# Kernel optimization log

Hardware: AMD Instinct MI355X
Metric: run time of the kernel (lower is better)

## Reference

```python
import jax, jax.numpy as jnp
import numpy as np

N, E, D_IN, H = 40000, 640000, 128, 128
R, B = 8, 30  # num_relations = 2*n_speakers**2, num_bases


def setup_inputs() -> dict:
    key = jax.random.key(0)
    ks = jax.random.split(key, 10)
    node_features = jax.random.normal(ks[0], (N, D_IN), jnp.float32)
    edge_index = jax.random.randint(ks[1], (2, E), 0, N)
    edge_type = jax.random.randint(ks[2], (E,), 0, R)
    edge_norm = jax.random.uniform(ks[3], (E,), jnp.float32)
    s_in = 1.0 / np.sqrt(D_IN)
    s_h = 1.0 / np.sqrt(H)
    basis = jax.random.normal(ks[4], (B, D_IN, H), jnp.float32) * s_in
    comp = jax.random.normal(ks[5], (R, B), jnp.float32) * (1.0 / np.sqrt(B))
    root = jax.random.normal(ks[6], (D_IN, H), jnp.float32) * s_in
    bias1 = jnp.zeros((H,), jnp.float32)
    w_rel = jax.random.normal(ks[7], (H, H), jnp.float32) * s_h
    w_root2 = jax.random.normal(ks[8], (H, H), jnp.float32) * s_h
    bias2 = jnp.zeros((H,), jnp.float32)
    return dict(node_features=node_features, edge_index=edge_index,
                edge_norm=edge_norm, edge_type=edge_type,
                basis=basis, comp=comp, root=root, bias1=bias1,
                w_rel=w_rel, w_root2=w_root2, bias2=bias2)


def reference(node_features, edge_index, edge_norm, edge_type,
              basis, comp, root, bias1, w_rel, w_root2, bias2):
    n = node_features.shape[0]
    src, dst = edge_index[0], edge_index[1]  # messages flow src -> dst

    # ---- RGCNConv (basis decomposition, mean aggregation, root + bias) ----
    # Per-relation weights from bases: [R, D_in, H]
    w = jnp.einsum('rb,bio->rio', comp, basis)
    # Transform all nodes by every relation once (avoids per-edge matmul): [R, N, H]
    xw = jnp.einsum('nd,rdo->rno', node_features, w)
    msgs = xw[edge_type, src]                                  # [E, H]
    agg = jax.ops.segment_sum(msgs, dst, num_segments=n)       # [N, H]
    deg = jax.ops.segment_sum(jnp.ones_like(dst, dtype=node_features.dtype),
                              dst, num_segments=n)
    agg = agg / jnp.maximum(deg, 1.0)[:, None]                 # mean aggregation
    h = agg + node_features @ root + bias1                     # [N, H]

    # ---- GraphConv (add aggregation): W_rel * sum_j x_j + W_root * x_i + b ----
    nbr = jax.ops.segment_sum(h[src], dst, num_segments=n)     # [N, H]
    out = nbr @ w_rel + h @ w_root2 + bias2
    return out
```

## Files before the change

### kernel.cpp

```cpp
#include <hip/hip_runtime.h>
#include <stdint.h>

#define DH 128
#define NB 30
#define NR 8

typedef short bf16x8 __attribute__((ext_vector_type(8)));
typedef float f32x4 __attribute__((ext_vector_type(4)));
typedef float f32x2 __attribute__((ext_vector_type(2)));

static __device__ __forceinline__ unsigned short f2bf(float f) {
    unsigned u = __float_as_uint(f);
    u += 0x7fffu + ((u >> 16) & 1u);
    return (unsigned short)(u >> 16);
}
static __device__ __forceinline__ float bflo(unsigned u) { return __uint_as_float(u << 16); }
static __device__ __forceinline__ float bfhi(unsigned u) { return __uint_as_float(u & 0xffff0000u); }

__global__ __launch_bounds__(256) void k_cvtx(const float* __restrict__ x,
                                              unsigned short* __restrict__ xbf, int n4) {
    int i = blockIdx.x * blockDim.x + threadIdx.x;
    if (i < n4) {
        float4 v = ((const float4*)x)[i];
        ushort4 u;
        u.x = f2bf(v.x); u.y = f2bf(v.y); u.z = f2bf(v.z); u.w = f2bf(v.w);
        ((ushort4*)xbf)[i] = u;
    }
}

__global__ __launch_bounds__(128) void k_wprep(const float* __restrict__ comp,
                                               const float* __restrict__ basis,
                                               const float* __restrict__ root,
                                               const float* __restrict__ wrel,
                                               const float* __restrict__ wroot2,
                                               unsigned short* __restrict__ wallT,
                                               unsigned short* __restrict__ WT2) {
    int o = threadIdx.x;
    int i = blockIdx.x;
    int y = blockIdx.y;
    if (y < NR) {
        float s = 0.f;
        #pragma unroll
        for (int b = 0; b < NB; ++b)
            s += comp[y * NB + b] * basis[((size_t)b * DH + i) * DH + o];
        wallT[((size_t)y * DH + o) * DH + i] = f2bf(s);
    } else if (y == NR) {
        wallT[((size_t)NR * DH + o) * DH + i] = f2bf(root[i * DH + o]);
    } else {
        const float* W = (y == NR + 2) ? wroot2 : wrel;
        WT2[((size_t)(y - NR - 1) * DH + o) * DH + i] = f2bf(W[i * DH + o]);
    }
}

__global__ void k_hist(const int* __restrict__ dst, int E, int* __restrict__ deg) {
    int e = blockIdx.x * blockDim.x + threadIdx.x;
    if (e < E) atomicAdd(&deg[dst[e]], 1);
}

__global__ __launch_bounds__(1024) void k_scan1(const int* __restrict__ deg, int n, int total_n,
                                                int* __restrict__ offsets, int* __restrict__ partial) {
    __shared__ int s[1024];
    int tid = threadIdx.x;
    int i = blockIdx.x * 1024 + tid;
    int v = (i < n) ? deg[i] : 0;
    s[tid] = v;
    __syncthreads();
    for (int off = 1; off < 1024; off <<= 1) {
        int t = (tid >= off) ? s[tid - off] : 0;
        __syncthreads();
        s[tid] += t;
        __syncthreads();
    }
    if (i < total_n) offsets[i] = s[tid] - v;
    if (tid == 1023) partial[blockIdx.x] = s[1023];
}

__global__ void k_scan2(int* __restrict__ partial, int nb) {
    if (threadIdx.x == 0) {
        int run = 0;
        for (int b = 0; b < nb; ++b) { int t = partial[b]; partial[b] = run; run += t; }
    }
}

__global__ __launch_bounds__(1024) void k_scan3(int* __restrict__ offsets,
                                                const int* __restrict__ partial, int total_n) {
    int i = blockIdx.x * 1024 + threadIdx.x;
    if (i < total_n) offsets[i] += partial[blockIdx.x];
}

__global__ void k_scatter(const int* __restrict__ src, const int* __restrict__ dstA,
                          const int* __restrict__ etype, int E,
                          const int* __restrict__ offsets, int* __restrict__ cursor,
                          unsigned* __restrict__ sorted) {
    int e = blockIdx.x * blockDim.x + threadIdx.x;
    if (e >= E) return;
    int d = dstA[e];
    int pos = offsets[d] + atomicAdd(&cursor[d], 1);
    sorted[pos] = (unsigned)src[e] | ((unsigned)etype[e] << 17);
}

__global__ __launch_bounds__(256) void k_gemm1m(const unsigned short* __restrict__ Xbf,
                                                const unsigned short* __restrict__ wallT,
                                                const float* __restrict__ bias1,
                                                int Nn,
                                                unsigned* __restrict__ xw8,
                                                unsigned short* __restrict__ hb) {
    __shared__ __align__(16) unsigned short As[128][136];
    __shared__ __align__(16) unsigned short Bs[128][136];
    const int tid = threadIdx.x;
    const int wave = tid >> 6, lane = tid & 63;
    const int g = blockIdx.y;
    const int rowbase = blockIdx.x * 128;
    const int lq = lane >> 4, lr = lane & 15;

    #pragma unroll
    for (int it = 0; it < 8; ++it) {
        int c = it * 256 + tid;
        int row = c >> 4, col = c & 15;
        int rg = rowbase + row; if (rg >= Nn) rg = Nn - 1;
        *(uint4*)&As[row][col * 8] = *(const uint4*)&Xbf[(size_t)rg * DH + col * 8];
    }

    for (int rr = 0; rr < 3; ++rr) {
        const int r = g * 3 + rr;
        const unsigned short* WT = wallT + (size_t)r * DH * DH;
        if (rr) __syncthreads();
        #pragma unroll
        for (int it = 0; it < 8; ++it) {
            int c = it * 256 + tid;
            int row = c >> 4, col = c & 15;
            *(uint4*)&Bs[row][col * 8] = *(const uint4*)&WT[(size_t)row * DH + col * 8];
        }
        __syncthreads();

        f32x4 acc[2][8];
        #pragma unroll
        for (int mt = 0; mt < 2; ++mt)
            #pragma unroll
            for (int nt = 0; nt < 8; ++nt) acc[mt][nt] = (f32x4)0.f;

        #pragma unroll
        for (int ks = 0; ks < 4; ++ks) {
            const int ko = ks * 32 + lq * 8;
            bf16x8 a0 = *(const bf16x8*)&As[wave * 32 + lr][ko];
            bf16x8 a1 = *(const bf16x8*)&As[wave * 32 + 16 + lr][ko];
            #pragma unroll
            for (int nt = 0; nt < 8; ++nt) {
                bf16x8 b = *(const bf16x8*)&Bs[nt * 16 + lr][ko];
                acc[0][nt] = __builtin_amdgcn_mfma_f32_16x16x32_bf16(a0, b, acc[0][nt], 0, 0, 0);
                acc[1][nt] = __builtin_amdgcn_mfma_f32_16x16x32_bf16(a1, b, acc[1][nt], 0, 0, 0);
            }
        }
        __syncthreads();

        float bv[8];
        #pragma unroll
        for (int nt = 0; nt < 8; ++nt) bv[nt] = (r == NR) ? bias1[nt * 16 + lr] : 0.f;
        #pragma unroll
        for (int mt = 0; mt < 2; ++mt)
            #pragma unroll
            for (int nt = 0; nt < 8; ++nt)
                #pragma unroll
                for (int reg = 0; reg < 4; ++reg) {
                    int ml = wave * 32 + mt * 16 + lq * 4 + reg;
                    Bs[ml][nt * 16 + lr] = f2bf(acc[mt][nt][reg] + bv[nt]);
                }
        __syncthreads();

        if (r < NR) {
            unsigned* dst = xw8 + ((size_t)r * Nn + rowbase) * (DH / 4);
            #pragma unroll
            for (int it = 0; it < 8; ++it) {
                int c = it * 256 + tid;
                int row = c >> 4, col = c & 15;
                if (rowbase + row < Nn) {
                    uint4 q = *(uint4*)&Bs[row][col * 8];
                    uint2 o;
                    o.x = __builtin_amdgcn_cvt_pk_fp8_f32(bflo(q.x), bfhi(q.x), 0, false);
                    o.x = __builtin_amdgcn_cvt_pk_fp8_f32(bflo(q.y), bfhi(q.y), o.x, true);
                    o.y = __builtin_amdgcn_cvt_pk_fp8_f32(bflo(q.z), bfhi(q.z), 0, false);
                    o.y = __builtin_amdgcn_cvt_pk_fp8_f32(bflo(q.w), bfhi(q.w), o.y, true);
                    *(uint2*)&dst[(size_t)row * (DH / 4) + col * 2] = o;
                }
            }
        } else {
            #pragma unroll
            for (int it = 0; it < 8; ++it) {
                int c = it * 256 + tid;
                int row = c >> 4, col = c & 15;
                if (rowbase + row < Nn)
                    *(uint4*)&hb[((size_t)(rowbase + row)) * DH + col * 8] = *(uint4*)&Bs[row][col * 8];
            }
        }
    }
}

__global__ __launch_bounds__(256) void k_agg1(const int* __restrict__ offsets,
                                              const unsigned* __restrict__ sorted,
                                              const unsigned* __restrict__ xw8,
                                              const unsigned* __restrict__ hb32,
                                              int Nn, unsigned* __restrict__ hbf) {
    int w = (blockIdx.x * blockDim.x + threadIdx.x) >> 6;
    if (w >= Nn) return;
    int lane = threadIdx.x & 63;
    int half = lane >> 5, sub = lane & 31;
    int s = offsets[w], e = offsets[w + 1];
    float a0 = 0.f, a1 = 0.f, a2 = 0.f, a3 = 0.f;
    for (int p = s; p < e; p += 16) {
        unsigned pk[8]; float m[8];
        #pragma unroll
        for (int j = 0; j < 8; ++j) {
            int q = p + 2 * j + half; bool v = q < e;
            pk[j] = sorted[v ? q : e - 1];
            m[j] = v ? 1.f : 0.f;
        }
        unsigned u[8];
        #pragma unroll
        for (int j = 0; j < 8; ++j)
            u[j] = xw8[((size_t)(pk[j] >> 17) * Nn + (pk[j] & 0x1FFFFu)) * 32 + sub];
        #pragma unroll
        for (int j = 0; j < 8; ++j) {
            f32x2 lo = __builtin_amdgcn_cvt_pk_f32_fp8(u[j], false);
            f32x2 hi = __builtin_amdgcn_cvt_pk_f32_fp8(u[j], true);
            a0 = fmaf(m[j], lo.x, a0);
            a1 = fmaf(m[j], lo.y, a1);
            a2 = fmaf(m[j], hi.x, a2);
            a3 = fmaf(m[j], hi.y, a3);
        }
    }
    a0 += __shfl_xor(a0, 32, 64);
    a1 += __shfl_xor(a1, 32, 64);
    a2 += __shfl_xor(a2, 32, 64);
    a3 += __shfl_xor(a3, 32, 64);
    if (half == 0) {
        float invd = 1.0f / fmaxf((float)(e - s), 1.0f);
        uint2 hv = *(const uint2*)&hb32[(size_t)w * 64 + sub * 2];
        float h0 = bflo(hv.x) + a0 * invd;
        float h1 = bfhi(hv.x) + a1 * invd;
        float h2 = bflo(hv.y) + a2 * invd;
        float h3 = bfhi(hv.y) + a3 * invd;
        uint2 o;
        o.x = (unsigned)f2bf(h0) | ((unsigned)f2bf(h1) << 16);
        o.y = (unsigned)f2bf(h2) | ((unsigned)f2bf(h3) << 16);
        *(uint2*)&hbf[(size_t)w * 64 + sub * 2] = o;
    }
}

__global__ __launch_bounds__(256) void k_agg2(const int* __restrict__ offsets,
                                              const unsigned* __restrict__ sorted,
                                              const unsigned* __restrict__ hbf32,
                                              int Nn, unsigned* __restrict__ nbrbf) {
    int w = (blockIdx.x * blockDim.x + threadIdx.x) >> 6;
    if (w >= Nn) return;
    int lane = threadIdx.x & 63;
    int s = offsets[w], e = offsets[w + 1];
    float ax = 0.f, ay = 0.f;
    for (int p = s; p < e; p += 16) {
        unsigned pk[16]; float m[16];
        #pragma unroll
        for (int j = 0; j < 16; ++j) {
            int q = p + j; bool v = q < e;
            pk[j] = sorted[v ? q : e - 1];
            m[j] = v ? 1.f : 0.f;
        }
        unsigned u[16];
        #pragma unroll
        for (int j = 0; j < 16; ++j)
            u[j] = hbf32[(size_t)(pk[j] & 0x1FFFFu) * 64 + lane];
        #pragma unroll
        for (int j = 0; j < 16; ++j) {
            ax = fmaf(m[j], __uint_as_float(u[j] << 16), ax);
            ay = fmaf(m[j], __uint_as_float(u[j] & 0xffff0000u), ay);
        }
    }
    nbrbf[(size_t)w * 64 + lane] = (unsigned)f2bf(ax) | ((unsigned)f2bf(ay) << 16);
}

__global__ __launch_bounds__(256) void k_gemm2m(const unsigned short* __restrict__ nbrbf,
                                                const unsigned short* __restrict__ hbf,
                                                const unsigned short* __restrict__ WT2,
                                                const float* __restrict__ bias2,
                                                int Nn, float* __restrict__ out) {
    __shared__ __align__(16) unsigned short As[128][136];
    __shared__ __align__(16) unsigned short Bs[128][136];
    const int tid = threadIdx.x;
    const int wave = tid >> 6, lane = tid & 63;
    const int rowbase = blockIdx.x * 128;
    const int lq = lane >> 4, lr = lane & 15;

    f32x4 acc[2][8];
    #pragma unroll
    for (int mt = 0; mt < 2; ++mt)
        #pragma unroll
        for (int nt = 0; nt < 8; ++nt) acc[mt][nt] = (f32x4)0.f;

    for (int ph = 0; ph < 2; ++ph) {
        const unsigned short* A = ph ? hbf : nbrbf;
        const unsigned short* WT = WT2 + (size_t)ph * DH * DH;
        if (ph) __syncthreads();
        #pragma unroll
        for (int it = 0; it < 8; ++it) {
            int c = it * 256 + tid;
            int row = c >> 4, col = c & 15;
            int rg = rowbase + row; if (rg >= Nn) rg = Nn - 1;
            *(uint4*)&As[row][col * 8] = *(const uint4*)&A[(size_t)rg * DH + col * 8];
            *(uint4*)&Bs[row][col * 8] = *(const uint4*)&WT[(size_t)row * DH + col * 8];
        }
        __syncthreads();
        #pragma unroll
        for (int ks = 0; ks < 4; ++ks) {
            const int ko = ks * 32 + lq * 8;
            bf16x8 a0 = *(const bf16x8*)&As[wave * 32 + lr][ko];
            bf16x8 a1 = *(const bf16x8*)&As[wave * 32 + 16 + lr][ko];
            #pragma unroll
            for (int nt = 0; nt < 8; ++nt) {
                bf16x8 b = *(const bf16x8*)&Bs[nt * 16 + lr][ko];
                acc[0][nt] = __builtin_amdgcn_mfma_f32_16x16x32_bf16(a0, b, acc[0][nt], 0, 0, 0);
                acc[1][nt] = __builtin_amdgcn_mfma_f32_16x16x32_bf16(a1, b, acc[1][nt], 0, 0, 0);
            }
        }
    }

    float bv[8];
    #pragma unroll
    for (int nt = 0; nt < 8; ++nt) bv[nt] = bias2[nt * 16 + lr];
    #pragma unroll
    for (int mt = 0; mt < 2; ++mt)
        #pragma unroll
        for (int nt = 0; nt < 8; ++nt)
            #pragma unroll
            for (int reg = 0; reg < 4; ++reg) {
                int m = rowbase + wave * 32 + mt * 16 + lq * 4 + reg;
                if (m < Nn) out[(size_t)m * DH + nt * 16 + lr] = acc[mt][nt][reg] + bv[nt];
            }
}

extern "C" void kernel_launch(void* const* d_in, const int* in_sizes, int n_in,
                              void* d_out, int out_size, void* d_ws, size_t ws_size,
                              hipStream_t stream) {
    const float* x      = (const float*)d_in[0];
    const int*   eidx   = (const int*)d_in[1];
    const int*   etype  = (const int*)d_in[3];
    const float* basis  = (const float*)d_in[4];
    const float* comp   = (const float*)d_in[5];
    const float* root   = (const float*)d_in[6];
    const float* bias1  = (const float*)d_in[7];
    const float* wrel   = (const float*)d_in[8];
    const float* wroot2 = (const float*)d_in[9];
    const float* bias2  = (const float*)d_in[10];
    float* out = (float*)d_out;

    const int N = in_sizes[0] / DH;
    const int E = in_sizes[3];
    const int* srcA = eidx;
    const int* dstA = eidx + E;

    char* ws = (char*)d_ws;
    size_t off = 0;
    auto alloc = [&](size_t bytes) -> void* {
        void* p = (void*)(ws + off);
        off += (bytes + 255) & ~(size_t)255;
        return p;
    };
    int* deg           = (int*)alloc((size_t)N * 4);
    int* cursor        = (int*)alloc((size_t)N * 4);
    int* offsets       = (int*)alloc((size_t)(N + 1) * 4);
    int* partial       = (int*)alloc(256 * 4);
    unsigned* sorted   = (unsigned*)alloc((size_t)E * 4);
    unsigned short* wallT = (unsigned short*)alloc((size_t)(NR + 1) * DH * DH * 2);
    unsigned short* WT2   = (unsigned short*)alloc((size_t)2 * DH * DH * 2);
    unsigned short* Xbf   = (unsigned short*)alloc((size_t)N * DH * 2);
    unsigned* xw8      = (unsigned*)alloc((size_t)NR * N * DH);
    unsigned short* hb = (unsigned short*)alloc((size_t)N * DH * 2);
    unsigned* hbf      = (unsigned*)alloc((size_t)N * (DH / 2) * 4);
    unsigned* nbrbf    = (unsigned*)alloc((size_t)N * (DH / 2) * 4);
    (void)ws_size; (void)n_in; (void)out_size;

    hipMemsetAsync(deg, 0, (size_t)N * 8, stream);

    k_cvtx<<<(N * DH / 4 + 255) / 256, 256, 0, stream>>>(x, Xbf, N * DH / 4);
    k_wprep<<<dim3(DH, NR + 3), DH, 0, stream>>>(comp, basis, root, wrel, wroot2, wallT, WT2);
    k_hist<<<(E + 255) / 256, 256, 0, stream>>>(dstA, E, deg);

    const int totn = N + 1;
    const int nsb = (totn + 1023) / 1024;
    k_scan1<<<nsb, 1024, 0, stream>>>(deg, N, totn, offsets, partial);
    k_scan2<<<1, 64, 0, stream>>>(partial, nsb);
    k_scan3<<<nsb, 1024, 0, stream>>>(offsets, partial, totn);
    k_scatter<<<(E + 255) / 256, 256, 0, stream>>>(srcA, dstA, etype, E, offsets, cursor, sorted);

    const int gx = (N + 127) / 128;
    k_gemm1m<<<dim3(gx, 3), 256, 0, stream>>>(Xbf, wallT, bias1, N, xw8, hb);
    k_agg1<<<(N * 64) / 256, 256, 0, stream>>>(offsets, sorted, xw8,
                                               (const unsigned*)hb, N, hbf);
    k_agg2<<<(N * 64) / 256, 256, 0, stream>>>(offsets, sorted, hbf, N, nbrbf);
    k_gemm2m<<<gx, 256, 0, stream>>>((const unsigned short*)nbrbf, (const unsigned short*)hbf,
                                     WT2, bias2, N, out);
}
```

Measured before the change: 252.4 us.

## Fuse CSR build into one cooperative kernel and fold bf16 conversion into GEMM

Replaces the histogram, three-stage scan and scatter kernels with one cooperative kernel that uses grid-wide syncs between phases. It also drops the separate fp32-to-bf16 conversion of node features and converts while loading tiles in the first GEMM. This targets launch overhead and an extra pass over x. The trade-offs are that the cooperative kernel uses only 40 blocks for the edge-wide atomic phases, and the GEMM now reads fp32 x once per relation group.

```diff
diff --git a/kernel.cpp b/kernel.cpp
--- a/kernel.cpp
+++ b/kernel.cpp
@@ -1,5 +1,8 @@
 #include <hip/hip_runtime.h>
+#include <hip/hip_cooperative_groups.h>
 #include <stdint.h>
+
+namespace cg = cooperative_groups;
 
 #define DH 128
 #define NB 30
@@ -16,17 +19,6 @@
 }
 static __device__ __forceinline__ float bflo(unsigned u) { return __uint_as_float(u << 16); }
 static __device__ __forceinline__ float bfhi(unsigned u) { return __uint_as_float(u & 0xffff0000u); }
-
-__global__ __launch_bounds__(256) void k_cvtx(const float* __restrict__ x,
-                                              unsigned short* __restrict__ xbf, int n4) {
-    int i = blockIdx.x * blockDim.x + threadIdx.x;
-    if (i < n4) {
-        float4 v = ((const float4*)x)[i];
-        ushort4 u;
-        u.x = f2bf(v.x); u.y = f2bf(v.y); u.z = f2bf(v.z); u.w = f2bf(v.w);
-        ((ushort4*)xbf)[i] = u;
-    }
-}
 
 __global__ __launch_bounds__(128) void k_wprep(const float* __restrict__ comp,
                                                const float* __restrict__ basis,
@@ -52,16 +44,26 @@
     }
 }
 
-__global__ void k_hist(const int* __restrict__ dst, int E, int* __restrict__ deg) {
-    int e = blockIdx.x * blockDim.x + threadIdx.x;
-    if (e < E) atomicAdd(&deg[dst[e]], 1);
-}
-
-__global__ __launch_bounds__(1024) void k_scan1(const int* __restrict__ deg, int n, int total_n,
-                                                int* __restrict__ offsets, int* __restrict__ partial) {
+__global__ __launch_bounds__(1024) void k_csr(const int* __restrict__ src,
+                                              const int* __restrict__ dstA,
+                                              const int* __restrict__ etype, int E,
+                                              int* __restrict__ deg,
+                                              int* __restrict__ offsets,
+                                              int* __restrict__ partial,
+                                              int* __restrict__ cursor,
+                                              unsigned* __restrict__ sorted, int n) {
+    cg::grid_group grid = cg::this_grid();
     __shared__ int s[1024];
-    int tid = threadIdx.x;
-    int i = blockIdx.x * 1024 + tid;
+    __shared__ int pre_s;
+    const int tid = threadIdx.x;
+    const int b = blockIdx.x;
+    const int T = gridDim.x * 1024;
+    const int gtid = b * 1024 + tid;
+
+    for (int e = gtid; e < E; e += T) atomicAdd(&deg[dstA[e]], 1);
+    grid.sync();
+
+    int i = b * 1024 + tid;
     int v = (i < n) ? deg[i] : 0;
     s[tid] = v;
     __syncthreads();
@@ -71,35 +73,27 @@
         s[tid] += t;
         __syncthreads();
     }
-    if (i < total_n) offsets[i] = s[tid] - v;
-    if (tid == 1023) partial[blockIdx.x] = s[1023];
-}
-
-__global__ void k_scan2(int* __restrict__ partial, int nb) {
-    if (threadIdx.x == 0) {
-        int run = 0;
-        for (int b = 0; b < nb; ++b) { int t = partial[b]; partial[b] = run; run += t; }
-    }
-}
-
-__global__ __launch_bounds__(1024) void k_scan3(int* __restrict__ offsets,
-                                                const int* __restrict__ partial, int total_n) {
-    int i = blockIdx.x * 1024 + threadIdx.x;
-    if (i < total_n) offsets[i] += partial[blockIdx.x];
-}
-
-__global__ void k_scatter(const int* __restrict__ src, const int* __restrict__ dstA,
-                          const int* __restrict__ etype, int E,
-                          const int* __restrict__ offsets, int* __restrict__ cursor,
-                          unsigned* __restrict__ sorted) {
-    int e = blockIdx.x * blockDim.x + threadIdx.x;
-    if (e >= E) return;
-    int d = dstA[e];
-    int pos = offsets[d] + atomicAdd(&cursor[d], 1);
-    sorted[pos] = (unsigned)src[e] | ((unsigned)etype[e] << 17);
-}
-
-__global__ __launch_bounds__(256) void k_gemm1m(const unsigned short* __restrict__ Xbf,
+    if (i <= n) offsets[i] = s[tid] - v;
+    if (tid == 1023) partial[b] = s[1023];
+    grid.sync();
+
+    if (tid == 0) {
+        int pre = 0;
+        for (int t = 0; t < b; ++t) pre += partial[t];
+        pre_s = pre;
+    }
+    __syncthreads();
+    if (i <= n) offsets[i] += pre_s;
+    grid.sync();
+
+    for (int e = gtid; e < E; e += T) {
+        int d = dstA[e];
+        int pos = offsets[d] + atomicAdd(&cursor[d], 1);
+        sorted[pos] = (unsigned)src[e] | ((unsigned)etype[e] << 17);
+    }
+}
+
+__global__ __launch_bounds__(256) void k_gemm1m(const float* __restrict__ x,
                                                 const unsigned short* __restrict__ wallT,
                                                 const float* __restrict__ bias1,
                                                 int Nn,
@@ -118,7 +112,14 @@
         int c = it * 256 + tid;
         int row = c >> 4, col = c & 15;
         int rg = rowbase + row; if (rg >= Nn) rg = Nn - 1;
-        *(uint4*)&As[row][col * 8] = *(const uint4*)&Xbf[(size_t)rg * DH + col * 8];
+        float4 v0 = *(const float4*)&x[(size_t)rg * DH + col * 8];
+        float4 v1 = *(const float4*)&x[(size_t)rg * DH + col * 8 + 4];
+        uint4 u;
+        u.x = (unsigned)f2bf(v0.x) | ((unsigned)f2bf(v0.y) << 16);
+        u.y = (unsigned)f2bf(v0.z) | ((unsigned)f2bf(v0.w) << 16);
+        u.z = (unsigned)f2bf(v1.x) | ((unsigned)f2bf(v1.y) << 16);
+        u.w = (unsigned)f2bf(v1.z) | ((unsigned)f2bf(v1.w) << 16);
+        *(uint4*)&As[row][col * 8] = u;
     }
 
     for (int rr = 0; rr < 3; ++rr) {
@@ -369,7 +370,6 @@
     unsigned* sorted   = (unsigned*)alloc((size_t)E * 4);
     unsigned short* wallT = (unsigned short*)alloc((size_t)(NR + 1) * DH * DH * 2);
     unsigned short* WT2   = (unsigned short*)alloc((size_t)2 * DH * DH * 2);
-    unsigned short* Xbf   = (unsigned short*)alloc((size_t)N * DH * 2);
     unsigned* xw8      = (unsigned*)alloc((size_t)NR * N * DH);
     unsigned short* hb = (unsigned short*)alloc((size_t)N * DH * 2);
     unsigned* hbf      = (unsigned*)alloc((size_t)N * (DH / 2) * 4);
@@ -378,19 +378,17 @@
 
     hipMemsetAsync(deg, 0, (size_t)N * 8, stream);
 
-    k_cvtx<<<(N * DH / 4 + 255) / 256, 256, 0, stream>>>(x, Xbf, N * DH / 4);
     k_wprep<<<dim3(DH, NR + 3), DH, 0, stream>>>(comp, basis, root, wrel, wroot2, wallT, WT2);
-    k_hist<<<(E + 255) / 256, 256, 0, stream>>>(dstA, E, deg);
-
-    const int totn = N + 1;
-    const int nsb = (totn + 1023) / 1024;
-    k_scan1<<<nsb, 1024, 0, stream>>>(deg, N, totn, offsets, partial);
-    k_scan2<<<1, 64, 0, stream>>>(partial, nsb);
-    k_scan3<<<nsb, 1024, 0, stream>>>(offsets, partial, totn);
-    k_scatter<<<(E + 255) / 256, 256, 0, stream>>>(srcA, dstA, etype, E, offsets, cursor, sorted);
+
+    {
+        void* args[] = {(void*)&srcA, (void*)&dstA, (void*)&etype, (void*)&E,
+                        (void*)&deg, (void*)&offsets, (void*)&partial,
+                        (void*)&cursor, (void*)&sorted, (void*)&N};
+        hipLaunchCooperativeKernel((const void*)k_csr, dim3(40), dim3(1024), args, 0, stream);
+    }
 
     const int gx = (N + 127) / 128;
-    k_gemm1m<<<dim3(gx, 3), 256, 0, stream>>>(Xbf, wallT, bias1, N, xw8, hb);
+    k_gemm1m<<<dim3(gx, 3), 256, 0, stream>>>(x, wallT, bias1, N, xw8, hb);
     k_agg1<<<(N * 64) / 256, 256, 0, stream>>>(offsets, sorted, xw8,
                                                (const unsigned*)hb, N, hbf);
     k_agg2<<<(N * 64) / 256, 256, 0, stream>>>(offsets, sorted, hbf, N, nbrbf);
```

Result: slower. 343.5 us (+36.1%).
